# Performance work log

Hardware: AMD Instinct MI355X
Metric: run time of the kernel (lower is better)

## Reference

```python
import jax, jax.numpy as jnp
import numpy as np

HIDDEN = 512

def flip_sequences(x, lengths):
    # flax sst2-style flip: reverse each sequence's first `length` items, padding stays at end
    B, T = x.shape[0], x.shape[1]
    idxs = (jnp.arange(T - 1, -1, -1)[None, :] + lengths[:, None]) % T  # [B,T]
    return x[jnp.arange(B)[:, None], idxs]

def lstm_scan(x, Wi, Wh, b):
    # x: [B,T,D] -> outputs [B,T,H]; flax OptimizedLSTMCell math (gate order i,f,g,o)
    B = x.shape[0]
    H = Wh.shape[0]
    xW = jnp.einsum('btd,dg->tbg', x, Wi) + b  # precompute input projections, time-major [T,B,4H]
    def step(carry, xw):
        c, h = carry
        gates = xw + h @ Wh
        i, f, g, o = jnp.split(gates, 4, axis=-1)
        c = jax.nn.sigmoid(f) * c + jax.nn.sigmoid(i) * jnp.tanh(g)
        h = jax.nn.sigmoid(o) * jnp.tanh(c)
        return (c, h), h
    init = (jnp.zeros((B, H), x.dtype), jnp.zeros((B, H), x.dtype))
    _, hs = jax.lax.scan(step, init, xW)  # hs: [T,B,H]
    return jnp.swapaxes(hs, 0, 1)

def setup_inputs() -> dict:
    key = jax.random.key(0)
    ks = jax.random.split(key, 8)
    B, T, D, H = 16, 2048, 512, HIDDEN
    s_in = 1.0 / np.sqrt(D)
    s_h = 1.0 / np.sqrt(H)
    return {
        'inputs': jax.random.normal(ks[0], (B, T, D), jnp.float32),
        'lengths': jax.random.randint(ks[1], (B,), 1, T + 1, jnp.int32),
        'Wi_f': jax.random.normal(ks[2], (D, 4 * H), jnp.float32) * s_in,
        'Wh_f': jax.random.normal(ks[3], (H, 4 * H), jnp.float32) * s_h,
        'b_f': jnp.zeros((4 * H,), jnp.float32),
        'Wi_b': jax.random.normal(ks[4], (D, 4 * H), jnp.float32) * s_in,
        'Wh_b': jax.random.normal(ks[5], (H, 4 * H), jnp.float32) * s_h,
        'b_b': jnp.zeros((4 * H,), jnp.float32),
    }

def reference(inputs, lengths, Wi_f, Wh_f, b_f, Wi_b, Wh_b, b_b):
    fwd = lstm_scan(inputs, Wi_f, Wh_f, b_f)  # [B,T,H]
    rev_in = flip_sequences(inputs, lengths)
    bwd = lstm_scan(rev_in, Wi_b, Wh_b, b_b)
    bwd = flip_sequences(bwd, lengths)
    return jnp.concatenate([fwd, bwd], axis=-1)  # [B,T,2H]
```

## Files before the change

kernel.cpp:

```cpp
#include <hip/hip_runtime.h>
#include <cstdint>
#include <cstddef>

#define T_SEQ 2048
#define BATCH 16
#define DIM   512
#define HID   512
#define NCOL  2048
#define XROW  520

typedef __attribute__((ext_vector_type(8))) short          s8v;
typedef __attribute__((ext_vector_type(4))) float          f4v;
typedef __attribute__((ext_vector_type(4))) unsigned short h4v;

#define HXBASE(d, s) (((size_t)((d) * 2 + (s)) * BATCH) * HID)

__device__ __forceinline__ unsigned short f2b(float f) {
  unsigned u = __builtin_bit_cast(unsigned, f);
  return (unsigned short)((u + 0x7fffu + ((u >> 16) & 1u)) >> 16);
}

#define MFMA16(a, w, c) __builtin_amdgcn_mfma_f32_16x16x32_bf16((a), (w), (c), 0, 0, 0)

__global__ __launch_bounds__(256, 1)
void lstm_persist(const float* __restrict__ x, const int* __restrict__ lengths,
                  const float* __restrict__ Wi_f, const float* __restrict__ Wh_f,
                  const float* __restrict__ b_f,
                  const float* __restrict__ Wi_b, const float* __restrict__ Wh_b,
                  const float* __restrict__ b_b,
                  unsigned int* __restrict__ hx,
                  float* __restrict__ out) {
  __shared__ unsigned short Ax[2][BATCH][XROW];
  __shared__ unsigned short Ah[BATCH][XROW];
  __shared__ float glds[4][BATCH][16];

  const int w    = (int)blockIdx.x;
  const int dir  = w >> 5;
  const int j0   = (w & 31) * 16;
  const int tid  = (int)threadIdx.x;
  const int lane = tid & 63;
  const int wv   = tid >> 6;

  const int b   = tid >> 4;
  const int sub = tid & 15;
  const int len = lengths[b];

  const float* bias = dir ? b_b : b_f;
  const float bi = bias[0 * HID + j0 + sub];
  const float bf = bias[1 * HID + j0 + sub];
  const float bg = bias[2 * HID + j0 + sub];
  const float bo = bias[3 * HID + j0 + sub];

  s8v wfi[16], wfh[16];
  {
    const float* Wi = dir ? Wi_b : Wi_f;
    const float* Wh = dir ? Wh_b : Wh_f;
    const int col = wv * HID + j0 + (lane & 15);
    const int kb  = (lane >> 4) * 8;
#pragma unroll
    for (int kc = 0; kc < 16; ++kc) {
      const float* src = Wi + (size_t)(kc * 32 + kb) * NCOL + col;
      s8v f;
#pragma unroll
      for (int j = 0; j < 8; ++j) f[j] = (short)f2b(src[(size_t)j * NCOL]);
      wfi[kc] = f;
    }
#pragma unroll
    for (int kc = 0; kc < 16; ++kc) {
      const float* src = Wh + (size_t)(kc * 32 + kb) * NCOL + col;
      s8v f;
#pragma unroll
      for (int j = 0; j < 8; ++j) f[j] = (short)f2b(src[(size_t)j * NCOL]);
      wfh[kc] = f;
    }
  }

  const int arow = lane & 15;
  const int koff = (lane >> 4) * 8;

  auto taus = [len, dir](int s) { return dir ? ((T_SEQ - 1 - s + len) & (T_SEQ - 1)) : s; };

  {
    const float* x0 = x + ((size_t)b * T_SEQ + taus(0)) * DIM;
    const float* x1 = x + ((size_t)b * T_SEQ + taus(1)) * DIM;
#pragma unroll
    for (int r = 0; r < 8; ++r) {
      const int k = sub * 4 + r * 64;
      f4v v0 = *(const f4v*)(x0 + k);
      f4v v1 = *(const f4v*)(x1 + k);
      h4v p0; p0[0] = f2b(v0[0]); p0[1] = f2b(v0[1]); p0[2] = f2b(v0[2]); p0[3] = f2b(v0[3]);
      h4v p1; p1[0] = f2b(v1[0]); p1[1] = f2b(v1[1]); p1[2] = f2b(v1[2]); p1[3] = f2b(v1[3]);
      *(h4v*)&Ax[0][b][k] = p0;
      *(h4v*)&Ax[1][b][k] = p1;
    }
  }
  __syncthreads();

  f4v accx;
  {
    f4v d0 = {0,0,0,0}, d1 = {0,0,0,0}, d2 = {0,0,0,0}, d3 = {0,0,0,0};
    const unsigned short* ap = &Ax[0][arow][koff];
#pragma unroll
    for (int kc = 0; kc < 16; kc += 4) {
      d0 = MFMA16(*(const s8v*)(ap + (kc + 0) * 32), wfi[kc + 0], d0);
      d1 = MFMA16(*(const s8v*)(ap + (kc + 1) * 32), wfi[kc + 1], d1);
      d2 = MFMA16(*(const s8v*)(ap + (kc + 2) * 32), wfi[kc + 2], d2);
      d3 = MFMA16(*(const s8v*)(ap + (kc + 3) * 32), wfi[kc + 3], d3);
    }
    accx = (d0 + d1) + (d2 + d3);
  }

  float c_state = 0.f;

  for (int t = 0; t < T_SEQ; ++t) {
    const unsigned e = (unsigned)(t + 1);
    const bool notlast = (t + 1 < T_SEQ);

    f4v xv[8];
    if (t + 2 < T_SEQ) {
      const float* xr = x + ((size_t)b * T_SEQ + taus(t + 2)) * DIM;
#pragma unroll
      for (int r = 0; r < 8; ++r) xv[r] = *(const f4v*)(xr + sub * 4 + r * 64);
    }

    f4v acc;
    {
      f4v d0 = accx, d1 = {0,0,0,0}, d2 = {0,0,0,0}, d3 = {0,0,0,0};
      if (t > 0) {
        const unsigned short* ap = &Ah[arow][koff];
#pragma unroll
        for (int kc = 0; kc < 16; kc += 4) {
          d0 = MFMA16(*(const s8v*)(ap + (kc + 0) * 32), wfh[kc + 0], d0);
          d1 = MFMA16(*(const s8v*)(ap + (kc + 1) * 32), wfh[kc + 1], d1);
          d2 = MFMA16(*(const s8v*)(ap + (kc + 2) * 32), wfh[kc + 2], d2);
          d3 = MFMA16(*(const s8v*)(ap + (kc + 3) * 32), wfh[kc + 3], d3);
        }
      }
      acc = (d0 + d1) + (d2 + d3);
    }
#pragma unroll
    for (int r = 0; r < 4; ++r)
      glds[wv][(lane >> 4) * 4 + r][lane & 15] = acc[r];
    __syncthreads();

    {
      const float gi = glds[0][b][sub] + bi;
      const float gf = glds[1][b][sub] + bf;
      const float gg = glds[2][b][sub] + bg;
      const float go = glds[3][b][sub] + bo;
      const float si = 1.f / (1.f + __expf(-gi));
      const float sf = 1.f / (1.f + __expf(-gf));
      const float so = 1.f / (1.f + __expf(-go));
      const float tg = 1.f - 2.f / (1.f + __expf(2.f * gg));
      c_state = sf * c_state + si * tg;
      const float tc = 1.f - 2.f / (1.f + __expf(2.f * c_state));
      const float h = so * tc;
      if (notlast) {
        const unsigned tagged = ((unsigned)f2b(h) << 16) | e;
        __hip_atomic_store(&hx[HXBASE(dir, e & 1) + (size_t)b * HID + j0 + sub], tagged,
                           __ATOMIC_RELAXED, __HIP_MEMORY_SCOPE_AGENT);
      }
      const int tauo = dir ? ((T_SEQ - 1 - t + len) & (T_SEQ - 1)) : t;
      out[((size_t)b * T_SEQ + tauo) * (2 * HID) + (size_t)dir * HID + j0 + sub] = h;
    }

    if (!notlast) break;

    const unsigned* hrow = hx + HXBASE(dir, e & 1) + (size_t)b * HID;
    unsigned long long hu[16];
#pragma unroll
    for (int r = 0; r < 8; ++r) {
      const int k = sub * 4 + r * 64;
      hu[2*r]   = __hip_atomic_load((const unsigned long long*)(hrow + k),
                                    __ATOMIC_RELAXED, __HIP_MEMORY_SCOPE_AGENT);
      hu[2*r+1] = __hip_atomic_load((const unsigned long long*)(hrow + k) + 1,
                                    __ATOMIC_RELAXED, __HIP_MEMORY_SCOPE_AGENT);
    }

    {
      f4v d0 = {0,0,0,0}, d1 = {0,0,0,0}, d2 = {0,0,0,0}, d3 = {0,0,0,0};
      const unsigned short* ap = &Ax[(t + 1) & 1][arow][koff];
#pragma unroll
      for (int kc = 0; kc < 16; kc += 4) {
        d0 = MFMA16(*(const s8v*)(ap + (kc + 0) * 32), wfi[kc + 0], d0);
        d1 = MFMA16(*(const s8v*)(ap + (kc + 1) * 32), wfi[kc + 1], d1);
        d2 = MFMA16(*(const s8v*)(ap + (kc + 2) * 32), wfi[kc + 2], d2);
        d3 = MFMA16(*(const s8v*)(ap + (kc + 3) * 32), wfi[kc + 3], d3);
      }
      accx = (d0 + d1) + (d2 + d3);
    }

    if (t + 2 < T_SEQ) {
#pragma unroll
      for (int r = 0; r < 8; ++r) {
        const int k = sub * 4 + r * 64;
        h4v p; p[0] = f2b(xv[r][0]); p[1] = f2b(xv[r][1]);
               p[2] = f2b(xv[r][2]); p[3] = f2b(xv[r][3]);
        *(h4v*)&Ax[t & 1][b][k] = p;
      }
    }

    {
      const unsigned long long msk = 0x0000FFFF0000FFFFULL;
      const unsigned long long pat = ((unsigned long long)e << 32) | e;
      int guard = 0;
      while (true) {
        bool ok = true;
#pragma unroll
        for (int r = 0; r < 16; ++r) ok &= ((hu[r] & msk) == pat);
        if (ok | (++guard > (1 << 14))) break;
        __builtin_amdgcn_s_sleep(1);
#pragma unroll
        for (int r = 0; r < 8; ++r) {
          const int k = sub * 4 + r * 64;
          hu[2*r]   = __hip_atomic_load((const unsigned long long*)(hrow + k),
                                        __ATOMIC_RELAXED, __HIP_MEMORY_SCOPE_AGENT);
          hu[2*r+1] = __hip_atomic_load((const unsigned long long*)(hrow + k) + 1,
                                        __ATOMIC_RELAXED, __HIP_MEMORY_SCOPE_AGENT);
        }
      }
    }

#pragma unroll
    for (int r = 0; r < 8; ++r) {
      const int k = sub * 4 + r * 64;
      h4v p;
      p[0] = (unsigned short)(hu[2*r]   >> 16);
      p[1] = (unsigned short)(hu[2*r]   >> 48);
      p[2] = (unsigned short)(hu[2*r+1] >> 16);
      p[3] = (unsigned short)(hu[2*r+1] >> 48);
      *(h4v*)&Ah[b][k] = p;
    }
    __syncthreads();
  }
}

extern "C" void kernel_launch(void* const* d_in, const int* in_sizes, int n_in,
                              void* d_out, int out_size, void* d_ws, size_t ws_size,
                              hipStream_t stream) {
  const float* x    = (const float*)d_in[0];
  const int*   len  = (const int*)d_in[1];
  const float* Wi_f = (const float*)d_in[2];
  const float* Wh_f = (const float*)d_in[3];
  const float* b_f  = (const float*)d_in[4];
  const float* Wi_b = (const float*)d_in[5];
  const float* Wh_b = (const float*)d_in[6];
  const float* b_b  = (const float*)d_in[7];
  float* out = (float*)d_out;
  unsigned int* hx = (unsigned int*)d_ws;

  hipMemsetAsync(d_ws, 0, (size_t)2 * 2 * BATCH * HID * 4, stream);
  hipLaunchKernelGGL(lstm_persist, dim3(64), dim3(256), 0, stream,
                     x, len, Wi_f, Wh_f, b_f, Wi_b, Wh_b, b_b, hx, out);
}
```

Baseline: 5.908 ms.

## Move input-projection MFMAs into the gate step and defer global output store

Instead of computing the x·Wi projection for the next step during the spin-wait window, the kernel now only preloads the bf16 x fragments into registers and runs the x MFMAs together with the h·Wh MFMAs each step. The output store and the next x global load are moved after the h broadcast and poll issue, and the first poll retry skips the sleep. This reorders the critical path so the matrix work sits in a different place relative to the cross-block wait. The trade-off is more MFMA work on the serial path, in exchange for less latency between publishing h and starting the poll.

```diff
diff --git a/kernel.cpp b/kernel.cpp
--- a/kernel.cpp
+++ b/kernel.cpp
@@ -96,19 +96,10 @@
   }
   __syncthreads();
 
-  f4v accx;
-  {
-    f4v d0 = {0,0,0,0}, d1 = {0,0,0,0}, d2 = {0,0,0,0}, d3 = {0,0,0,0};
-    const unsigned short* ap = &Ax[0][arow][koff];
-#pragma unroll
-    for (int kc = 0; kc < 16; kc += 4) {
-      d0 = MFMA16(*(const s8v*)(ap + (kc + 0) * 32), wfi[kc + 0], d0);
-      d1 = MFMA16(*(const s8v*)(ap + (kc + 1) * 32), wfi[kc + 1], d1);
-      d2 = MFMA16(*(const s8v*)(ap + (kc + 2) * 32), wfi[kc + 2], d2);
-      d3 = MFMA16(*(const s8v*)(ap + (kc + 3) * 32), wfi[kc + 3], d3);
-    }
-    accx = (d0 + d1) + (d2 + d3);
-  }
+  s8v xf[16];
+#pragma unroll
+  for (int kc = 0; kc < 16; ++kc)
+    xf[kc] = *(const s8v*)(&Ax[0][arow][koff] + kc * 32);
 
   float c_state = 0.f;
 
@@ -116,16 +107,16 @@
     const unsigned e = (unsigned)(t + 1);
     const bool notlast = (t + 1 < T_SEQ);
 
-    f4v xv[8];
-    if (t + 2 < T_SEQ) {
-      const float* xr = x + ((size_t)b * T_SEQ + taus(t + 2)) * DIM;
-#pragma unroll
-      for (int r = 0; r < 8; ++r) xv[r] = *(const f4v*)(xr + sub * 4 + r * 64);
-    }
-
     f4v acc;
     {
-      f4v d0 = accx, d1 = {0,0,0,0}, d2 = {0,0,0,0}, d3 = {0,0,0,0};
+      f4v d0 = {0,0,0,0}, d1 = {0,0,0,0}, d2 = {0,0,0,0}, d3 = {0,0,0,0};
+#pragma unroll
+      for (int kc = 0; kc < 16; kc += 4) {
+        d0 = MFMA16(xf[kc + 0], wfi[kc + 0], d0);
+        d1 = MFMA16(xf[kc + 1], wfi[kc + 1], d1);
+        d2 = MFMA16(xf[kc + 2], wfi[kc + 2], d2);
+        d3 = MFMA16(xf[kc + 3], wfi[kc + 3], d3);
+      }
       if (t > 0) {
         const unsigned short* ap = &Ah[arow][koff];
 #pragma unroll
@@ -143,6 +134,7 @@
       glds[wv][(lane >> 4) * 4 + r][lane & 15] = acc[r];
     __syncthreads();
 
+    float h;
     {
       const float gi = glds[0][b][sub] + bi;
       const float gf = glds[1][b][sub] + bf;
@@ -154,17 +146,18 @@
       const float tg = 1.f - 2.f / (1.f + __expf(2.f * gg));
       c_state = sf * c_state + si * tg;
       const float tc = 1.f - 2.f / (1.f + __expf(2.f * c_state));
-      const float h = so * tc;
+      h = so * tc;
       if (notlast) {
         const unsigned tagged = ((unsigned)f2b(h) << 16) | e;
         __hip_atomic_store(&hx[HXBASE(dir, e & 1) + (size_t)b * HID + j0 + sub], tagged,
                            __ATOMIC_RELAXED, __HIP_MEMORY_SCOPE_AGENT);
       }
-      const int tauo = dir ? ((T_SEQ - 1 - t + len) & (T_SEQ - 1)) : t;
-      out[((size_t)b * T_SEQ + tauo) * (2 * HID) + (size_t)dir * HID + j0 + sub] = h;
-    }
-
-    if (!notlast) break;
+    }
+
+    if (!notlast) {
+      out[((size_t)b * T_SEQ + taus(t)) * (2 * HID) + (size_t)dir * HID + j0 + sub] = h;
+      break;
+    }
 
     const unsigned* hrow = hx + HXBASE(dir, e & 1) + (size_t)b * HID;
     unsigned long long hu[16];
@@ -177,20 +170,21 @@
                                     __ATOMIC_RELAXED, __HIP_MEMORY_SCOPE_AGENT);
     }
 
-    {
-      f4v d0 = {0,0,0,0}, d1 = {0,0,0,0}, d2 = {0,0,0,0}, d3 = {0,0,0,0};
-      const unsigned short* ap = &Ax[(t + 1) & 1][arow][koff];
-#pragma unroll
-      for (int kc = 0; kc < 16; kc += 4) {
-        d0 = MFMA16(*(const s8v*)(ap + (kc + 0) * 32), wfi[kc + 0], d0);
-        d1 = MFMA16(*(const s8v*)(ap + (kc + 1) * 32), wfi[kc + 1], d1);
-        d2 = MFMA16(*(const s8v*)(ap + (kc + 2) * 32), wfi[kc + 2], d2);
-        d3 = MFMA16(*(const s8v*)(ap + (kc + 3) * 32), wfi[kc + 3], d3);
-      }
-      accx = (d0 + d1) + (d2 + d3);
-    }
-
-    if (t + 2 < T_SEQ) {
+    out[((size_t)b * T_SEQ + taus(t)) * (2 * HID) + (size_t)dir * HID + j0 + sub] = h;
+
+    f4v xv[8];
+    const bool havex2 = (t + 2 < T_SEQ);
+    if (havex2) {
+      const float* xr = x + ((size_t)b * T_SEQ + taus(t + 2)) * DIM;
+#pragma unroll
+      for (int r = 0; r < 8; ++r) xv[r] = *(const f4v*)(xr + sub * 4 + r * 64);
+    }
+
+#pragma unroll
+    for (int kc = 0; kc < 16; ++kc)
+      xf[kc] = *(const s8v*)(&Ax[(t + 1) & 1][arow][koff] + kc * 32);
+
+    if (havex2) {
 #pragma unroll
       for (int r = 0; r < 8; ++r) {
         const int k = sub * 4 + r * 64;
@@ -209,7 +203,7 @@
 #pragma unroll
         for (int r = 0; r < 16; ++r) ok &= ((hu[r] & msk) == pat);
         if (ok | (++guard > (1 << 14))) break;
-        __builtin_amdgcn_s_sleep(1);
+        if (guard > 1) __builtin_amdgcn_s_sleep(1);
 #pragma unroll
         for (int r = 0; r < 8; ++r) {
           const int k = sub * 4 + r * 64;
```

Measured after the change: 8.311 ms. 1.41x slower.
